# Kernel optimization log

Hardware: AMD Instinct MI355X
Metric: run time of the kernel (lower is better)

## Reference

```python
import math
import jax, jax.numpy as jnp
import numpy as np

B, T, C = 4, 2048, 2048
H, HKV, D = 16, 4, 128
REP = H // HKV
EPS = 1e-6


def setup_inputs() -> dict:
    key = jax.random.key(0)
    ks = jax.random.split(key, 5)
    x = jax.random.normal(ks[0], (B, T, C), dtype=jnp.float32)
    # true RoPE angles: theta=10000
    inv_freq = 1.0 / (10000.0 ** (np.arange(0, D, 2, dtype=np.float32) / D))
    angles = np.arange(T, dtype=np.float32)[:, None] * inv_freq[None, :]  # (T, D//2)
    freqs_cis = jnp.asarray(np.stack([np.cos(angles), np.sin(angles)], axis=-1))  # (T, D//2, 2)
    s = 0.02
    Wq = jax.random.normal(ks[1], (C, H * D), dtype=jnp.float32) * s
    Wk = jax.random.normal(ks[2], (C, HKV * D), dtype=jnp.float32) * s
    Wv = jax.random.normal(ks[3], (C, HKV * D), dtype=jnp.float32) * s
    Wc = jax.random.normal(ks[4], (C, C), dtype=jnp.float32) * s
    return {"x": x, "freqs_cis": freqs_cis, "Wq": Wq, "Wk": Wk, "Wv": Wv, "Wc": Wc}


def _rmsnorm(t):
    # x * rsqrt(mean(x^2) + eps) over last dim, computed in fp32
    ms = jnp.mean(t.astype(jnp.float32) ** 2, axis=-1, keepdims=True)
    return t * jax.lax.rsqrt(ms + EPS).astype(t.dtype)


def _rope(t, cos, sin):
    # t: (B, T, h, D); cos/sin: (1, T, 1, D//2)
    tr = t.astype(jnp.float32).reshape(*t.shape[:-1], D // 2, 2)
    t0, t1 = tr[..., 0], tr[..., 1]
    out = jnp.stack([t0 * cos - t1 * sin, t0 * sin + t1 * cos], axis=-1)
    return out.reshape(t.shape).astype(t.dtype)


def reference(x, freqs_cis, Wq, Wk, Wv, Wc):
    q = (x @ Wq).reshape(B, T, H, D)
    k = (x @ Wk).reshape(B, T, HKV, D)
    v = (x @ Wv).reshape(B, T, HKV, D)
    q = _rmsnorm(q)
    k = _rmsnorm(k)
    cos = freqs_cis[:T, :, 0][None, :, None, :]
    sin = freqs_cis[:T, :, 1][None, :, None, :]
    q = _rope(q, cos, sin)
    k = _rope(k, cos, sin)
    # GQA: group query heads per kv head instead of materializing expanded K/V
    qg = q.reshape(B, T, HKV, REP, D)
    scores = jnp.einsum('bqhrd,bkhd->bhrqk', qg, k) * (1.0 / math.sqrt(D))
    causal = jnp.tril(jnp.ones((T, T), dtype=bool))
    scores = jnp.where(causal[None, None, None, :, :], scores, -jnp.inf)
    att = jax.nn.softmax(scores, axis=-1)
    y = jnp.einsum('bhrqk,bkhd->bqhrd', att, v).reshape(B, T, C)
    return y @ Wc
```

## Files before the change

kernel.cpp:

```cpp
#include <hip/hip_runtime.h>
#include <cstdint>

#define B_ 4
#define T_ 2048
#define C_ 2048
#define H_ 16
#define HKV_ 4
#define D_ 128

typedef unsigned short u16;
typedef __bf16 bf16x8 __attribute__((ext_vector_type(8)));
typedef float f32x4 __attribute__((ext_vector_type(4)));
typedef float f32x16 __attribute__((ext_vector_type(16)));

typedef __attribute__((address_space(1))) const void gvoid;
typedef __attribute__((address_space(3))) void lvoid;

static __device__ __forceinline__ void async_cp16(const u16* g, u16* l) {
  __builtin_amdgcn_global_load_lds((gvoid*)g, (lvoid*)l, 16, 0, 0);
}

static __device__ __forceinline__ u16 f2bf(float f) {
  unsigned int x = __builtin_bit_cast(unsigned int, f);
  x += 0x7fffu + ((x >> 16) & 1u);
  return (u16)(x >> 16);
}
static __device__ __forceinline__ float bf2f(u16 u) {
  unsigned int x = ((unsigned int)u) << 16;
  return __builtin_bit_cast(float, x);
}

__global__ void cast_x_kernel(const float* __restrict__ in, u16* __restrict__ out, int n4) {
  int i = blockIdx.x * blockDim.x + threadIdx.x;
  if (i >= n4) return;
  float4 v = ((const float4*)in)[i];
  ushort4 o;
  o.x = f2bf(v.x); o.y = f2bf(v.y); o.z = f2bf(v.z); o.w = f2bf(v.w);
  ((ushort4*)out)[i] = o;
}

__global__ void wtrans_all_kernel(const float* __restrict__ Wq, const float* __restrict__ Wk,
                                  const float* __restrict__ Wv, const float* __restrict__ Wc,
                                  u16* __restrict__ Wcat, u16* __restrict__ WcT) {
  __shared__ float tile[64][65];
  int tb = blockIdx.x;
  const float* W; u16* WT; int Nw, t;
  if (tb < 1024)      { W = Wq; WT = Wcat;                         Nw = 2048; t = tb; }
  else if (tb < 1280) { W = Wk; WT = Wcat + (size_t)2048 * 2048;   Nw = 512;  t = tb - 1024; }
  else if (tb < 1536) { W = Wv; WT = Wcat + (size_t)2560 * 2048;   Nw = 512;  t = tb - 1280; }
  else                { W = Wc; WT = WcT;                          Nw = 2048; t = tb - 1536; }
  int ntiles = Nw >> 6;
  int n0 = (t % ntiles) * 64, k0 = (t / ntiles) * 64;
  int tid = threadIdx.x;
#pragma unroll
  for (int i = 0; i < 16; i++) {
    int idx = i * 256 + tid;
    int r = idx >> 6, c = idx & 63;
    tile[r][c] = W[(size_t)(k0 + r) * Nw + n0 + c];
  }
  __syncthreads();
#pragma unroll
  for (int i = 0; i < 16; i++) {
    int idx = i * 256 + tid;
    int r = idx >> 6, c = idx & 63;
    WT[(size_t)(n0 + r) * 2048 + k0 + c] = f2bf(tile[c][r]);
  }
}

template <bool F32OUT>
__global__ __launch_bounds__(256) void gemm_bt(const u16* __restrict__ A, const u16* __restrict__ BT,
                                               void* __restrict__ Cout, int M, int N, int K) {
  __shared__ __align__(16) u16 As[128 * 64];
  __shared__ __align__(16) u16 Bs[128 * 64];
  int tid = threadIdx.x;
  int w = tid >> 6, lane = tid & 63, quad = lane >> 4, lo = lane & 15;
  int wm = w >> 1, wn = w & 1;
  int m0 = blockIdx.y * 128, n0 = blockIdx.x * 128;
  int srow = w * 32 + (lane >> 3);
  int schunk = lane & 7;
  int gchunk = schunk ^ (lane >> 3);
  f32x4 acc[4][4] = {};
  for (int k0 = 0; k0 < K; k0 += 64) {
#pragma unroll
    for (int c = 0; c < 4; c++) {
      int r = srow + c * 8;
      async_cp16(&A[(size_t)(m0 + r) * K + k0 + gchunk * 8], &As[r * 64 + schunk * 8]);
      async_cp16(&BT[(size_t)(n0 + r) * K + k0 + gchunk * 8], &Bs[r * 64 + schunk * 8]);
    }
    __syncthreads();
#pragma unroll
    for (int kk = 0; kk < 2; kk++) {
      bf16x8 af[4], bfr[4];
#pragma unroll
      for (int mt = 0; mt < 4; mt++) {
        int r = wm * 64 + mt * 16 + lo;
        af[mt] = *(const bf16x8*)(&As[r * 64 + (((kk * 4 + quad) ^ (lo & 7)) << 3)]);
      }
#pragma unroll
      for (int nt = 0; nt < 4; nt++) {
        int r = wn * 64 + nt * 16 + lo;
        bfr[nt] = *(const bf16x8*)(&Bs[r * 64 + (((kk * 4 + quad) ^ (lo & 7)) << 3)]);
      }
#pragma unroll
      for (int mt = 0; mt < 4; mt++)
#pragma unroll
        for (int nt = 0; nt < 4; nt++)
          acc[mt][nt] = __builtin_amdgcn_mfma_f32_16x16x32_bf16(af[mt], bfr[nt], acc[mt][nt], 0, 0, 0);
    }
    __syncthreads();
  }
#pragma unroll
  for (int mt = 0; mt < 4; mt++)
#pragma unroll
    for (int nt = 0; nt < 4; nt++)
#pragma unroll
      for (int r = 0; r < 4; r++) {
        int mg = m0 + wm * 64 + mt * 16 + quad * 4 + r;
        int ng = n0 + wn * 64 + nt * 16 + lo;
        float v = acc[mt][nt][r];
        if (F32OUT) ((float*)Cout)[(size_t)mg * N + ng] = v;
        else ((u16*)Cout)[(size_t)mg * N + ng] = f2bf(v);
      }
}

__global__ void rmsrope_kernel(const u16* __restrict__ in, const float* __restrict__ freqs,
                               u16* __restrict__ out, int heads, int instride, float outscale) {
  int w = threadIdx.x >> 6, lane = threadIdx.x & 63;
  int row = blockIdx.x * 4 + w;
  int hh = row % heads;
  int rest = row / heads;
  int t = rest % T_;
  int b = rest / T_;
  const u16* ip = in + (size_t)(b * T_ + t) * instride + hh * D_;
  unsigned pr = *(const unsigned*)(&ip[2 * lane]);
  float t0 = bf2f((u16)(pr & 0xffff)), t1 = bf2f((u16)(pr >> 16));
  float ss = t0 * t0 + t1 * t1;
#pragma unroll
  for (int off = 32; off > 0; off >>= 1) ss += __shfl_xor(ss, off, 64);
  float scale = rsqrtf(ss * (1.0f / 128.0f) + 1e-6f) * outscale;
  float2 cs = ((const float2*)freqs)[t * 64 + lane];
  float a = t0 * scale, c = t1 * scale;
  float o0 = a * cs.x - c * cs.y;
  float o1 = a * cs.y + c * cs.x;
  size_t ob = ((size_t)(b * heads + hh) * T_ + t) * D_ + 2 * lane;
  *(unsigned*)(&out[ob]) = ((unsigned)f2bf(o1) << 16) | (unsigned)f2bf(o0);
}

__global__ void vtrans_kernel(const u16* __restrict__ v, u16* __restrict__ vt) {
  __shared__ u16 tile[64][65];
  int bh = blockIdx.x;
  int b = bh >> 2, h = bh & 3;
  int t0 = blockIdx.y * 64, d0 = blockIdx.z * 64;
  const u16* base = v + (size_t)b * T_ * 3072 + h * D_;
  u16* obase = vt + (size_t)bh * D_ * T_;
  int tid = threadIdx.x;
#pragma unroll
  for (int i = 0; i < 16; i++) {
    int idx = i * 256 + tid, tr = idx >> 6, dc = idx & 63;
    tile[tr][dc] = base[(size_t)(t0 + tr) * 3072 + d0 + dc];
  }
  __syncthreads();
#pragma unroll
  for (int i = 0; i < 16; i++) {
    int idx = i * 256 + tid, dr = idx >> 6, tc = idx & 63;
    obase[(size_t)(d0 + dr) * T_ + t0 + tc] = tile[tc][dr];
  }
}

__global__ __launch_bounds__(256) void flash_kernel(const u16* __restrict__ qb, const u16* __restrict__ kb,
                                                    const u16* __restrict__ vb, u16* __restrict__ yb) {
  __shared__ __align__(16) u16 smem[17408];
  u16* Ks = smem;
  u16* Vs = smem + 8192;
  int bh = blockIdx.x;
  int b = bh >> 4, hq = bh & 15;
  int jp = blockIdx.y;
  int tid = threadIdx.x, w = tid >> 6, lane = tid & 63;
  int half = lane >> 5, lq = lane & 31;
  int bhkv = b * HKV_ + (hq >> 2);
  const u16* kbase = kb + (size_t)bhkv * T_ * D_;
  const u16* vbase = vb + (size_t)bhkv * D_ * T_;
  const float L2E = 1.4426950408889634f;
  const float N12 = -17.312340490667562f;

  int kchunk = lane & 15, krow0 = w * 16 + (lane >> 4);
  int vchunk = lane & 7, vrow0 = w * 32 + (lane >> 3);

  for (int ph = 0; ph < 2; ph++) {
    int qt = ph ? jp : (15 - jp);
    const u16* qbase = qb + ((size_t)bh * T_ + qt * 128) * D_;
    int qwave = qt * 128 + w * 32;

    bf16x8 qf[8];
#pragma unroll
    for (int ds = 0; ds < 8; ds++)
      qf[ds] = *(const bf16x8*)(&qbase[(w * 32 + lq) * D_ + ds * 16 + half * 8]);

    f32x16 oacc[4] = {};
    float l_part = 0.f;

    int ktmax = 2 * qt + 1;
    for (int kt = 0; kt <= ktmax; kt++) {
      const u16* ksrc = kbase + (size_t)(kt * 64) * D_;
      const u16* vsrc = vbase + kt * 64;
#pragma unroll
      for (int c = 0; c < 4; c++) {
        int r = krow0 + c * 4;
        async_cp16(&ksrc[r * D_ + ((kchunk ^ (r & 7)) << 3)], &Ks[r * 128 + (kchunk << 3)]);
      }
#pragma unroll
      for (int c = 0; c < 4; c++) {
        int r = vrow0 + c * 8;
        async_cp16(&vsrc[(size_t)r * T_ + ((vchunk ^ (r & 7)) << 3)], &Vs[r * 64 + (vchunk << 3)]);
      }
      __syncthreads();

#pragma unroll
      for (int t = 0; t < 2; t++) {
        int k0 = kt * 64 + t * 32;
        if (k0 > qwave + 31) continue;

        f32x16 s = {};
#pragma unroll
        for (int ds = 0; ds < 8; ds++) {
          bf16x8 kf = *(const bf16x8*)(&Ks[(t * 32 + lq) * 128 + ((((ds << 1) + half) ^ (lq & 7)) << 3)]);
          s = __builtin_amdgcn_mfma_f32_32x32x16_bf16(kf, qf[ds], s, 0, 0, 0);
        }

        int qglob = qwave + lq;
        if (k0 + 31 > qwave) {
#pragma unroll
          for (int i = 0; i < 16; i++) {
            int kl = k0 + 4 * half + (i & 3) + ((i >> 2) << 3);
            if (kl > qglob) s[i] = -1e30f;
          }
        }

        unsigned pd[8];
#pragma unroll
        for (int j2 = 0; j2 < 8; j2++) {
          float p0 = __builtin_amdgcn_exp2f(fmaf(s[2 * j2], L2E, N12));
          float p1 = __builtin_amdgcn_exp2f(fmaf(s[2 * j2 + 1], L2E, N12));
          l_part += p0 + p1;
          pd[j2] = __builtin_amdgcn_perm(__builtin_bit_cast(unsigned, p1),
                                         __builtin_bit_cast(unsigned, p0), 0x07060302u);
        }

        unsigned s0 = (unsigned)__shfl_xor((int)(half ? pd[0] : pd[2]), 32, 64);
        unsigned s1 = (unsigned)__shfl_xor((int)(half ? pd[1] : pd[3]), 32, 64);
        unsigned s2 = (unsigned)__shfl_xor((int)(half ? pd[4] : pd[6]), 32, 64);
        unsigned s3 = (unsigned)__shfl_xor((int)(half ? pd[5] : pd[7]), 32, 64);
        uint4 f0 = half ? uint4{s0, s1, pd[2], pd[3]} : uint4{pd[0], pd[1], s0, s1};
        uint4 f1 = half ? uint4{s2, s3, pd[6], pd[7]} : uint4{pd[4], pd[5], s2, s3};

#pragma unroll
        for (int kstep = 0; kstep < 2; kstep++) {
          uint4 fr = kstep ? f1 : f0;
          bf16x8 pf = __builtin_bit_cast(bf16x8, fr);
          int cR = (t * 2 + kstep) * 2 + half;
#pragma unroll
          for (int dt = 0; dt < 4; dt++) {
            bf16x8 vf = *(const bf16x8*)(&Vs[(dt * 32 + lq) * 64 + ((cR ^ (lq & 7)) << 3)]);
            oacc[dt] = __builtin_amdgcn_mfma_f32_32x32x16_bf16(vf, pf, oacc[dt], 0, 0, 0);
          }
        }
      }
      __syncthreads();
    }

    float lt = l_part + __shfl_xor(l_part, 32, 64);
    float inv = 1.0f / lt;

    u16* Ep = smem;
#pragma unroll
    for (int dt = 0; dt < 4; dt++)
#pragma unroll
      for (int j2 = 0; j2 < 8; j2++) {
        float p0 = oacc[dt][2 * j2] * inv;
        float p1 = oacc[dt][2 * j2 + 1] * inv;
        unsigned pk = ((unsigned)f2bf(p0)) | (((unsigned)f2bf(p1)) << 16);
        int d = dt * 32 + 4 * half + 2 * (j2 & 1) + ((j2 >> 1) << 3);
        *(unsigned*)(&Ep[(w * 32 + lq) * 136 + d]) = pk;
      }
    __syncthreads();

    int ic = tid & 15, qr0 = tid >> 4;
    size_t orow = ((size_t)b * T_ + qt * 128) * 2048 + hq * 128;
#pragma unroll
    for (int j2 = 0; j2 < 8; j2++) {
      int qr = qr0 + j2 * 16;
      uint4 v4 = *(const uint4*)(&Ep[qr * 136 + ic * 8]);
      *(uint4*)(&yb[orow + (size_t)qr * 2048 + ic * 8]) = v4;
    }
    __syncthreads();
  }
}

extern "C" void kernel_launch(void* const* d_in, const int* in_sizes, int n_in,
                              void* d_out, int out_size, void* d_ws, size_t ws_size,
                              hipStream_t stream) {
  const float* x = (const float*)d_in[0];
  const float* freqs = (const float*)d_in[1];
  const float* Wq = (const float*)d_in[2];
  const float* Wk = (const float*)d_in[3];
  const float* Wv = (const float*)d_in[4];
  const float* Wc = (const float*)d_in[5];
  float* out = (float*)d_out;

  char* ws = (char*)d_ws;
  size_t off = 0;
  auto alloc = [&](size_t bytes) { char* p = ws + off; off += (bytes + 255) & ~255ull; return p; };
  u16* xb   = (u16*)alloc((size_t)B_ * T_ * C_ * 2);
  u16* Wcat = (u16*)alloc((size_t)C_ * 3072 * 2);
  u16* WcT  = (u16*)alloc((size_t)C_ * C_ * 2);
  u16* qkvp = (u16*)alloc((size_t)B_ * T_ * 3072 * 2);
  u16* qb   = (u16*)alloc((size_t)B_ * H_ * T_ * D_ * 2);
  u16* kb   = (u16*)alloc((size_t)B_ * HKV_ * T_ * D_ * 2);
  u16* vb   = (u16*)alloc((size_t)B_ * HKV_ * T_ * D_ * 2);
  u16* yb   = (u16*)alloc((size_t)B_ * T_ * H_ * D_ * 2);

  cast_x_kernel<<<dim3(B_ * T_ * C_ / 1024), dim3(256), 0, stream>>>(x, xb, B_ * T_ * C_ / 4);
  wtrans_all_kernel<<<dim3(2560), dim3(256), 0, stream>>>(Wq, Wk, Wv, Wc, Wcat, WcT);

  gemm_bt<false><<<dim3(24, 64), dim3(256), 0, stream>>>(xb, Wcat, (void*)qkvp, 8192, 3072, 2048);

  const float sc = 0.08838834764831845f;
  rmsrope_kernel<<<dim3(B_ * T_ * H_ / 4), dim3(256), 0, stream>>>(qkvp, freqs, qb, H_, 3072, sc);
  rmsrope_kernel<<<dim3(B_ * T_ * HKV_ / 4), dim3(256), 0, stream>>>(qkvp + 2048, freqs, kb, HKV_, 3072, 1.0f);
  vtrans_kernel<<<dim3(16, 32, 2), dim3(256), 0, stream>>>(qkvp + 2560, vb);

  flash_kernel<<<dim3(B_ * H_, 8), dim3(256), 0, stream>>>(qb, kb, vb, yb);

  gemm_bt<true><<<dim3(16, 64), dim3(256), 0, stream>>>(yb, WcT, (void*)out, 8192, 2048, 2048);
}
```

Measured before the change: 478.9 us.

## Fuse RMSNorm, RoPE and V transpose into QKV GEMM epilogue; merge prep kernels

The QKV projection GEMM now performs RMSNorm, RoPE and the head-major scatter of Q/K in its epilogue. The norm is reduced across the two warps that share a row through shared memory, and the rotated tile is staged in LDS so stores are coalesced. V is written directly in transposed layout, and the x cast and weight transposes are merged into one launch. This removes the qkvp intermediate round trip, the separate rmsrope and vtrans launches, and a double bf16 rounding. In exchange the GEMM epilogue does more work, and the V stores are strided.

```diff
diff --git a/kernel.cpp b/kernel.cpp
--- a/kernel.cpp
+++ b/kernel.cpp
@@ -25,33 +25,33 @@
   x += 0x7fffu + ((x >> 16) & 1u);
   return (u16)(x >> 16);
 }
-static __device__ __forceinline__ float bf2f(u16 u) {
-  unsigned int x = ((unsigned int)u) << 16;
-  return __builtin_bit_cast(float, x);
-}
-
-__global__ void cast_x_kernel(const float* __restrict__ in, u16* __restrict__ out, int n4) {
-  int i = blockIdx.x * blockDim.x + threadIdx.x;
-  if (i >= n4) return;
-  float4 v = ((const float4*)in)[i];
-  ushort4 o;
-  o.x = f2bf(v.x); o.y = f2bf(v.y); o.z = f2bf(v.z); o.w = f2bf(v.w);
-  ((ushort4*)out)[i] = o;
-}
-
-__global__ void wtrans_all_kernel(const float* __restrict__ Wq, const float* __restrict__ Wk,
-                                  const float* __restrict__ Wv, const float* __restrict__ Wc,
-                                  u16* __restrict__ Wcat, u16* __restrict__ WcT) {
+
+__global__ void prep_kernel(const float* __restrict__ x, const float* __restrict__ Wq,
+                            const float* __restrict__ Wk, const float* __restrict__ Wv,
+                            const float* __restrict__ Wc, u16* __restrict__ xb,
+                            u16* __restrict__ Wcat, u16* __restrict__ WcT) {
   __shared__ float tile[64][65];
-  int tb = blockIdx.x;
+  int tb = blockIdx.x, tid = threadIdx.x;
+  if (tb < 4096) {
+    const float4* in4 = (const float4*)x;
+#pragma unroll
+    for (int j = 0; j < 4; j++) {
+      int i = tb * 1024 + j * 256 + tid;
+      float4 v = in4[i];
+      ushort4 o;
+      o.x = f2bf(v.x); o.y = f2bf(v.y); o.z = f2bf(v.z); o.w = f2bf(v.w);
+      ((ushort4*)xb)[i] = o;
+    }
+    return;
+  }
+  int tb2 = tb - 4096;
   const float* W; u16* WT; int Nw, t;
-  if (tb < 1024)      { W = Wq; WT = Wcat;                         Nw = 2048; t = tb; }
-  else if (tb < 1280) { W = Wk; WT = Wcat + (size_t)2048 * 2048;   Nw = 512;  t = tb - 1024; }
-  else if (tb < 1536) { W = Wv; WT = Wcat + (size_t)2560 * 2048;   Nw = 512;  t = tb - 1280; }
-  else                { W = Wc; WT = WcT;                          Nw = 2048; t = tb - 1536; }
+  if (tb2 < 1024)      { W = Wq; WT = Wcat;                       Nw = 2048; t = tb2; }
+  else if (tb2 < 1280) { W = Wk; WT = Wcat + (size_t)2048 * 2048; Nw = 512;  t = tb2 - 1024; }
+  else if (tb2 < 1536) { W = Wv; WT = Wcat + (size_t)2560 * 2048; Nw = 512;  t = tb2 - 1280; }
+  else                 { W = Wc; WT = WcT;                        Nw = 2048; t = tb2 - 1536; }
   int ntiles = Nw >> 6;
   int n0 = (t % ntiles) * 64, k0 = (t / ntiles) * 64;
-  int tid = threadIdx.x;
 #pragma unroll
   for (int i = 0; i < 16; i++) {
     int idx = i * 256 + tid;
@@ -67,9 +67,131 @@
   }
 }
 
-template <bool F32OUT>
+__global__ __launch_bounds__(256) void gemm_qkv_fused(const u16* __restrict__ xb, const u16* __restrict__ Wcat,
+                                                      const float* __restrict__ freqs,
+                                                      u16* __restrict__ qb, u16* __restrict__ kb,
+                                                      u16* __restrict__ vb) {
+  __shared__ __align__(16) char smem[35840];
+  u16* As = (u16*)smem;
+  u16* Bs = (u16*)(smem + 16384);
+  int tid = threadIdx.x;
+  int w = tid >> 6, lane = tid & 63, quad = lane >> 4, lo = lane & 15;
+  int wd = w >> 1, wt = w & 1;
+  int m0 = blockIdx.y * 128, n0 = blockIdx.x * 128;
+  int srow = w * 32 + (lane >> 3);
+  int schunk = lane & 7;
+  int gchunk = schunk ^ (lane >> 3);
+  f32x4 acc[4][4] = {};
+  for (int k0 = 0; k0 < 2048; k0 += 64) {
+#pragma unroll
+    for (int c = 0; c < 4; c++) {
+      int r = srow + c * 8;
+      async_cp16(&xb[(size_t)(m0 + r) * 2048 + k0 + gchunk * 8], &As[r * 64 + schunk * 8]);
+      async_cp16(&Wcat[(size_t)(n0 + r) * 2048 + k0 + gchunk * 8], &Bs[r * 64 + schunk * 8]);
+    }
+    __syncthreads();
+#pragma unroll
+    for (int kk = 0; kk < 2; kk++) {
+      bf16x8 wf[4], xf[4];
+#pragma unroll
+      for (int dt = 0; dt < 4; dt++) {
+        int r = wd * 64 + dt * 16 + lo;
+        wf[dt] = *(const bf16x8*)(&Bs[r * 64 + (((kk * 4 + quad) ^ (lo & 7)) << 3)]);
+      }
+#pragma unroll
+      for (int tt = 0; tt < 4; tt++) {
+        int r = wt * 64 + tt * 16 + lo;
+        xf[tt] = *(const bf16x8*)(&As[r * 64 + (((kk * 4 + quad) ^ (lo & 7)) << 3)]);
+      }
+#pragma unroll
+      for (int dt = 0; dt < 4; dt++)
+#pragma unroll
+        for (int tt = 0; tt < 4; tt++)
+          acc[dt][tt] = __builtin_amdgcn_mfma_f32_16x16x32_bf16(wf[dt], xf[tt], acc[dt][tt], 0, 0, 0);
+    }
+    __syncthreads();
+  }
+
+  if (n0 >= 2560) {
+    int head = (n0 - 2560) >> 7;
+#pragma unroll
+    for (int dt = 0; dt < 4; dt++)
+#pragma unroll
+      for (int tt = 0; tt < 4; tt++) {
+        int g = m0 + wt * 64 + tt * 16 + lo;
+        int b = g >> 11, t = g & 2047;
+        size_t base = ((size_t)(b * HKV_ + head) * D_) * T_ + t;
+#pragma unroll
+        for (int r = 0; r < 4; r++) {
+          int dd = wd * 64 + dt * 16 + quad * 4 + r;
+          vb[base + (size_t)dd * T_] = f2bf(acc[dt][tt][r]);
+        }
+      }
+    return;
+  }
+
+  int isQ = (n0 < 2048);
+  int head = isQ ? (n0 >> 7) : ((n0 - 2048) >> 7);
+  float* red = (float*)(smem + 34816);
+  float ss[4] = {0.f, 0.f, 0.f, 0.f};
+#pragma unroll
+  for (int tt = 0; tt < 4; tt++)
+#pragma unroll
+    for (int dt = 0; dt < 4; dt++)
+#pragma unroll
+      for (int r = 0; r < 4; r++) ss[tt] += acc[dt][tt][r] * acc[dt][tt][r];
+#pragma unroll
+  for (int tt = 0; tt < 4; tt++) {
+    ss[tt] += __shfl_xor(ss[tt], 16, 64);
+    ss[tt] += __shfl_xor(ss[tt], 32, 64);
+  }
+  if (quad == 0) {
+#pragma unroll
+    for (int tt = 0; tt < 4; tt++) red[(wt * 64 + tt * 16 + lo) * 2 + wd] = ss[tt];
+  }
+  __syncthreads();
+  float qs = isQ ? 0.08838834764831845f : 1.0f;
+  float scl[4];
+#pragma unroll
+  for (int tt = 0; tt < 4; tt++) {
+    int tl = wt * 64 + tt * 16 + lo;
+    scl[tt] = rsqrtf((red[tl * 2] + red[tl * 2 + 1]) * (1.0f / 128.0f) + 1e-6f) * qs;
+  }
+
+  u16* Tr = (u16*)smem;
+#pragma unroll
+  for (int tt = 0; tt < 4; tt++) {
+    int tl = wt * 64 + tt * 16 + lo;
+    int t = (m0 + tl) & 2047;
+#pragma unroll
+    for (int dt = 0; dt < 4; dt++) {
+      float4 f = *(const float4*)(freqs + (size_t)t * 128 + wd * 64 + dt * 16 + quad * 4);
+      float t0 = acc[dt][tt][0] * scl[tt], t1 = acc[dt][tt][1] * scl[tt];
+      unsigned pk0 = (unsigned)f2bf(t0 * f.x - t1 * f.y) | (((unsigned)f2bf(t0 * f.y + t1 * f.x)) << 16);
+      t0 = acc[dt][tt][2] * scl[tt]; t1 = acc[dt][tt][3] * scl[tt];
+      unsigned pk1 = (unsigned)f2bf(t0 * f.z - t1 * f.w) | (((unsigned)f2bf(t0 * f.w + t1 * f.z)) << 16);
+      int dd = wd * 64 + dt * 16 + quad * 4;
+      *(unsigned*)(&Tr[tl * 136 + dd]) = pk0;
+      *(unsigned*)(&Tr[tl * 136 + dd + 2]) = pk1;
+    }
+  }
+  __syncthreads();
+
+  u16* dst = isQ ? qb : kb;
+  int heads = isQ ? H_ : HKV_;
+  int seg = tid & 15, r0 = tid >> 4;
+#pragma unroll
+  for (int j = 0; j < 8; j++) {
+    int tl = r0 + j * 16;
+    int g = m0 + tl;
+    int b = g >> 11, t = g & 2047;
+    uint4 v4 = *(const uint4*)(&Tr[tl * 136 + seg * 8]);
+    *(uint4*)(&dst[((size_t)(b * heads + head) * T_ + t) * D_ + seg * 8]) = v4;
+  }
+}
+
 __global__ __launch_bounds__(256) void gemm_bt(const u16* __restrict__ A, const u16* __restrict__ BT,
-                                               void* __restrict__ Cout, int M, int N, int K) {
+                                               float* __restrict__ Cout, int M, int N, int K) {
   __shared__ __align__(16) u16 As[128 * 64];
   __shared__ __align__(16) u16 Bs[128 * 64];
   int tid = threadIdx.x;
@@ -117,54 +239,8 @@
       for (int r = 0; r < 4; r++) {
         int mg = m0 + wm * 64 + mt * 16 + quad * 4 + r;
         int ng = n0 + wn * 64 + nt * 16 + lo;
-        float v = acc[mt][nt][r];
-        if (F32OUT) ((float*)Cout)[(size_t)mg * N + ng] = v;
-        else ((u16*)Cout)[(size_t)mg * N + ng] = f2bf(v);
-      }
-}
-
-__global__ void rmsrope_kernel(const u16* __restrict__ in, const float* __restrict__ freqs,
-                               u16* __restrict__ out, int heads, int instride, float outscale) {
-  int w = threadIdx.x >> 6, lane = threadIdx.x & 63;
-  int row = blockIdx.x * 4 + w;
-  int hh = row % heads;
-  int rest = row / heads;
-  int t = rest % T_;
-  int b = rest / T_;
-  const u16* ip = in + (size_t)(b * T_ + t) * instride + hh * D_;
-  unsigned pr = *(const unsigned*)(&ip[2 * lane]);
-  float t0 = bf2f((u16)(pr & 0xffff)), t1 = bf2f((u16)(pr >> 16));
-  float ss = t0 * t0 + t1 * t1;
-#pragma unroll
-  for (int off = 32; off > 0; off >>= 1) ss += __shfl_xor(ss, off, 64);
-  float scale = rsqrtf(ss * (1.0f / 128.0f) + 1e-6f) * outscale;
-  float2 cs = ((const float2*)freqs)[t * 64 + lane];
-  float a = t0 * scale, c = t1 * scale;
-  float o0 = a * cs.x - c * cs.y;
-  float o1 = a * cs.y + c * cs.x;
-  size_t ob = ((size_t)(b * heads + hh) * T_ + t) * D_ + 2 * lane;
-  *(unsigned*)(&out[ob]) = ((unsigned)f2bf(o1) << 16) | (unsigned)f2bf(o0);
-}
-
-__global__ void vtrans_kernel(const u16* __restrict__ v, u16* __restrict__ vt) {
-  __shared__ u16 tile[64][65];
-  int bh = blockIdx.x;
-  int b = bh >> 2, h = bh & 3;
-  int t0 = blockIdx.y * 64, d0 = blockIdx.z * 64;
-  const u16* base = v + (size_t)b * T_ * 3072 + h * D_;
-  u16* obase = vt + (size_t)bh * D_ * T_;
-  int tid = threadIdx.x;
-#pragma unroll
-  for (int i = 0; i < 16; i++) {
-    int idx = i * 256 + tid, tr = idx >> 6, dc = idx & 63;
-    tile[tr][dc] = base[(size_t)(t0 + tr) * 3072 + d0 + dc];
-  }
-  __syncthreads();
-#pragma unroll
-  for (int i = 0; i < 16; i++) {
-    int idx = i * 256 + tid, dr = idx >> 6, tc = idx & 63;
-    obase[(size_t)(d0 + dr) * T_ + t0 + tc] = tile[tc][dr];
-  }
+        Cout[(size_t)mg * N + ng] = acc[mt][nt][r];
+      }
 }
 
 __global__ __launch_bounds__(256) void flash_kernel(const u16* __restrict__ qb, const u16* __restrict__ kb,
@@ -313,23 +389,13 @@
   u16* xb   = (u16*)alloc((size_t)B_ * T_ * C_ * 2);
   u16* Wcat = (u16*)alloc((size_t)C_ * 3072 * 2);
   u16* WcT  = (u16*)alloc((size_t)C_ * C_ * 2);
-  u16* qkvp = (u16*)alloc((size_t)B_ * T_ * 3072 * 2);
   u16* qb   = (u16*)alloc((size_t)B_ * H_ * T_ * D_ * 2);
   u16* kb   = (u16*)alloc((size_t)B_ * HKV_ * T_ * D_ * 2);
   u16* vb   = (u16*)alloc((size_t)B_ * HKV_ * T_ * D_ * 2);
   u16* yb   = (u16*)alloc((size_t)B_ * T_ * H_ * D_ * 2);
 
-  cast_x_kernel<<<dim3(B_ * T_ * C_ / 1024), dim3(256), 0, stream>>>(x, xb, B_ * T_ * C_ / 4);
-  wtrans_all_kernel<<<dim3(2560), dim3(256), 0, stream>>>(Wq, Wk, Wv, Wc, Wcat, WcT);
-
-  gemm_bt<false><<<dim3(24, 64), dim3(256), 0, stream>>>(xb, Wcat, (void*)qkvp, 8192, 3072, 2048);
-
-  const float sc = 0.08838834764831845f;
-  rmsrope_kernel<<<dim3(B_ * T_ * H_ / 4), dim3(256), 0, stream>>>(qkvp, freqs, qb, H_, 3072, sc);
-  rmsrope_kernel<<<dim3(B_ * T_ * HKV_ / 4), dim3(256), 0, stream>>>(qkvp + 2048, freqs, kb, HKV_, 3072, 1.0f);
-  vtrans_kernel<<<dim3(16, 32, 2), dim3(256), 0, stream>>>(qkvp + 2560, vb);
-
+  prep_kernel<<<dim3(4096 + 2560), dim3(256), 0, stream>>>(x, Wq, Wk, Wv, Wc, xb, Wcat, WcT);
+  gemm_qkv_fused<<<dim3(24, 64), dim3(256), 0, stream>>>(xb, Wcat, freqs, qb, kb, vb);
   flash_kernel<<<dim3(B_ * H_, 8), dim3(256), 0, stream>>>(qb, kb, vb, yb);
-
-  gemm_bt<true><<<dim3(16, 64), dim3(256), 0, stream>>>(yb, WcT, (void*)out, 8192, 2048, 2048);
-}
+  gemm_bt<<<dim3(16, 64), dim3(256), 0, stream>>>(yb, WcT, out, 8192, 2048, 2048);
+}
```

Result: faster. 465.1 us (-2.9%).
